# Performance work log

Hardware: AMD Instinct MI355X
Metric: run time of the kernel (lower is better)

The kernel has to match this reference:

```python
import jax, jax.numpy as jnp
import numpy as np

HIDDEN_DIM = 2048
CODE_DIM = 256
CODEBOOK_SIZE = 512
FC_DIMS = [1024, 512]
BATCH = 16384
EPS = 1e-5
NEG_SLOPE = 0.01  # PyTorch LeakyReLU default


def _linear_init(key, fan_in, fan_out):
    # kaiming_uniform_(a=sqrt(3)) ~= U(-1/sqrt(fan_in), 1/sqrt(fan_in)) scaled; use uniform bound
    bound = 1.0 / np.sqrt(fan_in)
    return jax.random.uniform(key, (fan_in, fan_out), jnp.float32, -bound, bound)


def setup_inputs() -> dict:
    key = jax.random.key(0)
    ks = jax.random.split(key, 16)
    h = jax.random.normal(ks[0], (BATCH, HIDDEN_DIM), jnp.float32)
    # encoder: Linear(2048->1024, no bias), BN, LReLU, Linear(1024->512, no bias), BN, LReLU, Linear(512->256, bias)
    enc_w1 = _linear_init(ks[1], HIDDEN_DIM, FC_DIMS[0])
    enc_bn1_g = jnp.ones((FC_DIMS[0],), jnp.float32)
    enc_bn1_b = jnp.zeros((FC_DIMS[0],), jnp.float32)
    enc_w2 = _linear_init(ks[2], FC_DIMS[0], FC_DIMS[1])
    enc_bn2_g = jnp.ones((FC_DIMS[1],), jnp.float32)
    enc_bn2_b = jnp.zeros((FC_DIMS[1],), jnp.float32)
    enc_w3 = _linear_init(ks[3], FC_DIMS[1], CODE_DIM)
    enc_b3 = jax.random.uniform(ks[4], (CODE_DIM,), jnp.float32, -1/np.sqrt(FC_DIMS[1]), 1/np.sqrt(FC_DIMS[1]))
    # codebook: NearestEmbed weight shape (code_dim, codebook_size)
    codebook = jax.random.normal(ks[5], (CODE_DIM, CODEBOOK_SIZE), jnp.float32)
    # decoder: Linear(256->512, no bias), BN, LReLU, Linear(512->1024, no bias), BN, LReLU, Linear(1024->2048, bias)
    dec_w1 = _linear_init(ks[6], CODE_DIM, FC_DIMS[1])
    dec_bn1_g = jnp.ones((FC_DIMS[1],), jnp.float32)
    dec_bn1_b = jnp.zeros((FC_DIMS[1],), jnp.float32)
    dec_w2 = _linear_init(ks[7], FC_DIMS[1], FC_DIMS[0])
    dec_bn2_g = jnp.ones((FC_DIMS[0],), jnp.float32)
    dec_bn2_b = jnp.zeros((FC_DIMS[0],), jnp.float32)
    dec_w3 = _linear_init(ks[8], FC_DIMS[0], HIDDEN_DIM)
    dec_b3 = jax.random.uniform(ks[9], (HIDDEN_DIM,), jnp.float32, -1/np.sqrt(FC_DIMS[0]), 1/np.sqrt(FC_DIMS[0]))
    return dict(h=h, enc_w1=enc_w1, enc_bn1_g=enc_bn1_g, enc_bn1_b=enc_bn1_b,
                enc_w2=enc_w2, enc_bn2_g=enc_bn2_g, enc_bn2_b=enc_bn2_b,
                enc_w3=enc_w3, enc_b3=enc_b3, codebook=codebook,
                dec_w1=dec_w1, dec_bn1_g=dec_bn1_g, dec_bn1_b=dec_bn1_b,
                dec_w2=dec_w2, dec_bn2_g=dec_bn2_g, dec_bn2_b=dec_bn2_b,
                dec_w3=dec_w3, dec_b3=dec_b3)


def _bn(x, g, b):
    # BatchNorm1d, training mode: biased batch variance, eps=1e-5
    mu = jnp.mean(x, axis=0)
    var = jnp.var(x, axis=0)
    return (x - mu) * jax.lax.rsqrt(var + EPS) * g + b


def _lrelu(x):
    return jnp.where(x >= 0, x, NEG_SLOPE * x)


def _quantize(z_e, codebook):
    # nearest codebook entry; codebook is [code_dim, K]
    # dist[b,k] = ||z_e[b] - codebook[:,k]||^2 (expanded, drop constant ||z||^2 for argmin? keep full for clarity)
    d = (jnp.sum(z_e * z_e, axis=1, keepdims=True)
         - 2.0 * (z_e @ codebook)
         + jnp.sum(codebook * codebook, axis=0)[None, :])  # [B, K]
    idx = jnp.argmin(d, axis=1)  # [B]
    z_q = codebook.T[idx]        # [B, code_dim]
    return z_q, idx


def reference(h, enc_w1, enc_bn1_g, enc_bn1_b, enc_w2, enc_bn2_g, enc_bn2_b,
              enc_w3, enc_b3, codebook,
              dec_w1, dec_bn1_g, dec_bn1_b, dec_w2, dec_bn2_g, dec_bn2_b,
              dec_w3, dec_b3):
    # encoder
    x = _lrelu(_bn(h @ enc_w1, enc_bn1_g, enc_bn1_b))
    x = _lrelu(_bn(x @ enc_w2, enc_bn2_g, enc_bn2_b))
    z_e = x @ enc_w3 + enc_b3  # [B, code_dim]
    # nearest-embed quantization with straight-through estimator
    z_q_raw, code_indices = _quantize(z_e, codebook)
    z_q = z_e + jax.lax.stop_gradient(z_q_raw - z_e)
    # decoder
    y = _lrelu(_bn(z_q @ dec_w1, dec_bn1_g, dec_bn1_b))
    y = _lrelu(_bn(y @ dec_w2, dec_bn2_g, dec_bn2_b))
    h_recon = y @ dec_w3 + dec_b3  # [B, hidden_dim]
    return z_e, z_q, h_recon, code_indices
```

## Files before the change

kernel.cpp:

```cpp
#include <hip/hip_runtime.h>
#include <hip/hip_fp16.h>
#include <cstdint>
#include <cstddef>

typedef _Float16 f16;
typedef _Float16 half8 __attribute__((ext_vector_type(8)));
typedef _Float16 half4 __attribute__((ext_vector_type(4)));
typedef float floatx4 __attribute__((ext_vector_type(4)));

static constexpr size_t NB  = 16384;
static constexpr size_t DH  = 2048;
static constexpr size_t F1  = 1024;
static constexpr size_t F2  = 512;
static constexpr size_t CD  = 256;
static constexpr size_t KCB = 512;

static constexpr size_t ZE_OFF  = 0;
static constexpr size_t ZQ_OFF  = NB * CD;
static constexpr size_t HR_OFF  = 2 * NB * CD;
static constexpr size_t IDX_OFF = 2 * NB * CD + NB * DH;

static constexpr size_t O_HH   = 0;
static constexpr size_t O_HL   = O_HH + NB * DH * 2;
static constexpr size_t R1_END = O_HL + NB * DH * 2;

static constexpr size_t R_X1H = 0;
static constexpr size_t R_X1L = NB * F1 * 2;
static constexpr size_t R_X2F = 2 * NB * F1 * 2;
static constexpr size_t R_X2H = R_X2F + NB * F2 * 4;
static constexpr size_t R_X2L = R_X2H + NB * F2 * 2;
static constexpr size_t R_Y1F = 0;
static constexpr size_t R_Y1H = NB * F2 * 4;
static constexpr size_t R_Y2H = 0;

static constexpr size_t O_W1H = R1_END;
static constexpr size_t O_W1L = O_W1H + F1 * DH * 2;
static constexpr size_t O_W2H = O_W1L + F1 * DH * 2;
static constexpr size_t O_W2L = O_W2H + F2 * F1 * 2;
static constexpr size_t O_W3H = O_W2L + F2 * F1 * 2;
static constexpr size_t O_W3L = O_W3H + CD * F2 * 2;
static constexpr size_t O_CBH = O_W3L + CD * F2 * 2;
static constexpr size_t O_CBL = O_CBH + KCB * CD * 2;
static constexpr size_t O_DW1 = O_CBL + KCB * CD * 2;
static constexpr size_t O_DW2 = O_DW1 + F2 * CD * 2;
static constexpr size_t O_DW3 = O_DW2 + F1 * F2 * 2;
static constexpr size_t O_SUM = O_DW3 + DH * F1 * 2;
static constexpr size_t O_SQ  = O_SUM + 4 * 1024 * 8;
static constexpr size_t O_SC  = O_SQ + 4 * 1024 * 8;
static constexpr size_t O_SH  = O_SC + 4 * 1024 * 4;
static constexpr size_t O_CN  = O_SH + 4 * 1024 * 4;
static constexpr size_t R2    = (O_CN + 4096 + 255) & ~(size_t)255;
static constexpr size_t R2_X1F = R2;
static constexpr size_t R2_ZEH = R2;
static constexpr size_t R2_ZEL = R2 + NB * CD * 2;
static constexpr size_t R2_S   = R2 + 2 * NB * CD * 2;
static constexpr size_t R2_ZQH = R2_S + NB * KCB * 4;
static constexpr size_t R2_Y2F = R2;

#define GLLDS(src, dst)                                                          \
    __builtin_amdgcn_global_load_lds(                                            \
        (const __attribute__((address_space(1))) void*)(src),                    \
        (__attribute__((address_space(3))) void*)(dst), 16, 0, 0)

#define VMCNT(n)  asm volatile("s_waitcnt vmcnt(" #n ")" ::: "memory")
#define LGKMCNT0  asm volatile("s_waitcnt lgkmcnt(0)" ::: "memory")

template<int MW, bool BIAS, bool STATS, bool WSPLIT>
__global__ __launch_bounds__(512)
void gemm3_t(const f16* __restrict__ Ah_, const f16* __restrict__ Al_,
             const f16* __restrict__ Bh_, const f16* __restrict__ Bl_,
             float* __restrict__ C, const float* __restrict__ bias,
             double* __restrict__ ssum, double* __restrict__ ssq,
             f16* __restrict__ zeh, f16* __restrict__ zel,
             int M, int N, int K)
{
    constexpr int BM = MW * 32;
    __shared__ f16 lds[2][2][16384];
    const int tid  = threadIdx.x;
    const int lane = tid & 63;
    const int w    = tid >> 6;
    const int wr   = w >> 2, wn = w & 3;
    const int row0 = blockIdx.x * BM;
    const int col0 = blockIdx.y * 256;

    const int rr8 = lane >> 3;
    const int p   = (lane & 7) ^ rr8;
    const int rr  = w * 32 + rr8;
    const int arr = rr & (BM - 1);
    const f16* srcH = (p < 4) ? (Ah_ + (size_t)(row0 + arr) * K + p * 8)
                              : (Bh_ + (size_t)(col0 + rr) * K + (p - 4) * 8);
    const f16* srcL = (p < 4) ? (Al_ + (size_t)(row0 + arr) * K + p * 8)
                              : (Bl_ + (size_t)(col0 + rr) * K + (p - 4) * 8);
    const int dstBase = w * 32 * 64;
    const int KT = K >> 5;

    floatx4 acc[MW][4];
#pragma unroll
    for (int m = 0; m < MW; ++m)
#pragma unroll
        for (int n = 0; n < 4; ++n)
#pragma unroll
            for (int j = 0; j < 4; ++j) acc[m][n][j] = 0.f;

    const int l15 = lane & 15;
    const int sA  = lane >> 4;

#pragma unroll
    for (int j = 0; j < 4; ++j)
        GLLDS(srcH + (size_t)j * 8 * K, &lds[0][0][dstBase + j * 512]);
#pragma unroll
    for (int j = 0; j < 4; ++j)
        GLLDS(srcL + (size_t)j * 8 * K, &lds[0][1][dstBase + j * 512]);
    VMCNT(4);
    __builtin_amdgcn_s_barrier();

    half8 afh[MW], afl[MW], bfh[4], bfl[4];

    for (int kt = 0; kt < KT; ++kt) {
        const int cur = kt & 1, nxt = cur ^ 1;
        const int koff = (kt + 1 < KT ? kt + 1 : kt) << 5;
        const f16* plH = lds[cur][0];
        const f16* plL = lds[cur][1];

#pragma unroll
        for (int m = 0; m < MW; ++m) {
            const int rA = wr * (MW * 16) + m * 16 + l15;
            afh[m] = *(const half8*)(plH + rA * 64 + (((sA) ^ (rA & 7)) << 3));
        }
#pragma unroll
        for (int n = 0; n < 4; ++n) {
            const int rB = wn * 64 + n * 16 + l15;
            bfh[n] = *(const half8*)(plH + rB * 64 + (((4 + sA) ^ (rB & 7)) << 3));
        }
#pragma unroll
        for (int j = 0; j < 4; ++j)
            GLLDS(srcH + (size_t)j * 8 * K + koff, &lds[nxt][0][dstBase + j * 512]);
        VMCNT(4);
        __builtin_amdgcn_s_barrier();
        LGKMCNT0;
        __builtin_amdgcn_sched_barrier(0);
        __builtin_amdgcn_s_setprio(1);
#pragma unroll
        for (int m = 0; m < MW; ++m)
#pragma unroll
            for (int n = 0; n < 4; ++n)
                acc[m][n] = __builtin_amdgcn_mfma_f32_16x16x32_f16(afh[m], bfh[n], acc[m][n], 0, 0, 0);
        __builtin_amdgcn_s_setprio(0);
        __builtin_amdgcn_s_barrier();

#pragma unroll
        for (int n = 0; n < 4; ++n) {
            const int rB = wn * 64 + n * 16 + l15;
            bfl[n] = *(const half8*)(plL + rB * 64 + (((4 + sA) ^ (rB & 7)) << 3));
        }
#pragma unroll
        for (int j = 0; j < 2; ++j)
            GLLDS(srcL + (size_t)j * 8 * K + koff, &lds[nxt][1][dstBase + j * 512]);
        __builtin_amdgcn_s_barrier();
        LGKMCNT0;
        __builtin_amdgcn_sched_barrier(0);
        __builtin_amdgcn_s_setprio(1);
#pragma unroll
        for (int m = 0; m < MW; ++m)
#pragma unroll
            for (int n = 0; n < 4; ++n)
                acc[m][n] = __builtin_amdgcn_mfma_f32_16x16x32_f16(afh[m], bfl[n], acc[m][n], 0, 0, 0);
        __builtin_amdgcn_s_setprio(0);
        __builtin_amdgcn_s_barrier();

#pragma unroll
        for (int m = 0; m < MW; ++m) {
            const int rA = wr * (MW * 16) + m * 16 + l15;
            afl[m] = *(const half8*)(plL + rA * 64 + (((sA) ^ (rA & 7)) << 3));
        }
#pragma unroll
        for (int j = 2; j < 4; ++j)
            GLLDS(srcL + (size_t)j * 8 * K + koff, &lds[nxt][1][dstBase + j * 512]);
        VMCNT(4);
        __builtin_amdgcn_s_barrier();
        LGKMCNT0;
        __builtin_amdgcn_sched_barrier(0);
        __builtin_amdgcn_s_setprio(1);
#pragma unroll
        for (int m = 0; m < MW; ++m)
#pragma unroll
            for (int n = 0; n < 4; ++n)
                acc[m][n] = __builtin_amdgcn_mfma_f32_16x16x32_f16(afl[m], bfh[n], acc[m][n], 0, 0, 0);
        __builtin_amdgcn_s_setprio(0);
        __builtin_amdgcn_s_barrier();
    }
    VMCNT(0);

    const int cb0 = col0 + wn * 64;
    const int rb0 = row0 + wr * (MW * 16) + (lane >> 4) * 4;
#pragma unroll
    for (int n = 0; n < 4; ++n) {
        const int col = cb0 + n * 16 + l15;
        const float bv = BIAS ? bias[col] : 0.f;
        double sd = 0.0, sq = 0.0;
#pragma unroll
        for (int m = 0; m < MW; ++m) {
            const int row = rb0 + m * 16;
#pragma unroll
            for (int j = 0; j < 4; ++j) {
                const float v = acc[m][n][j] + bv;
                const size_t o = (size_t)(row + j) * N + col;
                C[o] = v;
                if (WSPLIT) {
                    const f16 hv = (f16)v;
                    zeh[o] = hv;
                    zel[o] = (f16)(v - (float)hv);
                }
                if (STATS) { sd += (double)v; sq += (double)v * (double)v; }
            }
        }
        if (STATS) {
            sd += __shfl_xor(sd, 16);
            sd += __shfl_xor(sd, 32);
            sq += __shfl_xor(sq, 16);
            sq += __shfl_xor(sq, 32);
            if (lane < 16) {
                atomicAdd(ssum + col, sd);
                atomicAdd(ssq + col, sq);
            }
        }
    }
}

template<bool BIAS, bool STATS>
__global__ __launch_bounds__(512)
void gemm1_8ph(const f16* __restrict__ A_, const f16* __restrict__ B_,
               float* __restrict__ C, const float* __restrict__ bias,
               double* __restrict__ ssum, double* __restrict__ ssq,
               int M, int N, int K)
{
    __shared__ f16 lds[3][16384];
    const int tid  = threadIdx.x;
    const int lane = tid & 63;
    const int w    = tid >> 6;
    const int wr   = w >> 2, wn = w & 3;
    const int row0 = blockIdx.x * 256;
    const int col0 = blockIdx.y * 256;

    const int rr8 = lane >> 3;
    const int p   = (lane & 7) ^ rr8;
    const int rr  = w * 32 + rr8;
    const f16* srcH = (p < 4) ? (A_ + (size_t)(row0 + rr) * K + p * 8)
                              : (B_ + (size_t)(col0 + rr) * K + (p - 4) * 8);
    const int dstBase = w * 32 * 64;
    const int KT = K >> 5;

    floatx4 acc[8][4];
#pragma unroll
    for (int m = 0; m < 8; ++m)
#pragma unroll
        for (int n = 0; n < 4; ++n)
#pragma unroll
            for (int j = 0; j < 4; ++j) acc[m][n][j] = 0.f;

    const int l15 = lane & 15;
    const int sA  = lane >> 4;

#pragma unroll
    for (int j = 0; j < 4; ++j)
        GLLDS(srcH + (size_t)j * 8 * K, &lds[0][dstBase + j * 512]);
    {
        const int k1 = (KT > 1 ? 1 : 0) << 5;
#pragma unroll
        for (int j = 0; j < 4; ++j)
            GLLDS(srcH + (size_t)j * 8 * K + k1, &lds[1][dstBase + j * 512]);
    }
    VMCNT(4);
    __builtin_amdgcn_s_barrier();

    half8 afh[8], bfh[4];

    for (int kt = 0; kt < KT; ++kt) {
        const int cur = kt % 3, tgt = (kt + 2) % 3;
        const int koff = (kt + 2 < KT ? kt + 2 : KT - 1) << 5;
        const f16* plH = lds[cur];

#pragma unroll
        for (int m = 0; m < 8; ++m) {
            const int rA = wr * 128 + m * 16 + l15;
            afh[m] = *(const half8*)(plH + rA * 64 + (((sA) ^ (rA & 7)) << 3));
        }
#pragma unroll
        for (int n = 0; n < 4; ++n) {
            const int rB = wn * 64 + n * 16 + l15;
            bfh[n] = *(const half8*)(plH + rB * 64 + (((4 + sA) ^ (rB & 7)) << 3));
        }
#pragma unroll
        for (int j = 0; j < 2; ++j)
            GLLDS(srcH + (size_t)j * 8 * K + koff, &lds[tgt][dstBase + j * 512]);
        __builtin_amdgcn_s_barrier();
        LGKMCNT0;
        __builtin_amdgcn_sched_barrier(0);
        __builtin_amdgcn_s_setprio(1);
#pragma unroll
        for (int m = 0; m < 8; ++m)
#pragma unroll
            for (int n = 0; n < 2; ++n)
                acc[m][n] = __builtin_amdgcn_mfma_f32_16x16x32_f16(afh[m], bfh[n], acc[m][n], 0, 0, 0);
        __builtin_amdgcn_s_setprio(0);
        __builtin_amdgcn_s_barrier();

#pragma unroll
        for (int j = 2; j < 4; ++j)
            GLLDS(srcH + (size_t)j * 8 * K + koff, &lds[tgt][dstBase + j * 512]);
        VMCNT(4);
        __builtin_amdgcn_s_barrier();
        __builtin_amdgcn_s_setprio(1);
#pragma unroll
        for (int m = 0; m < 8; ++m)
#pragma unroll
            for (int n = 2; n < 4; ++n)
                acc[m][n] = __builtin_amdgcn_mfma_f32_16x16x32_f16(afh[m], bfh[n], acc[m][n], 0, 0, 0);
        __builtin_amdgcn_s_setprio(0);
        __builtin_amdgcn_s_barrier();
    }
    VMCNT(0);

    const int cb0 = col0 + wn * 64;
    const int rb0 = row0 + wr * 128 + (lane >> 4) * 4;
#pragma unroll
    for (int n = 0; n < 4; ++n) {
        const int col = cb0 + n * 16 + l15;
        const float bv = BIAS ? bias[col] : 0.f;
        double sd = 0.0, sq = 0.0;
#pragma unroll
        for (int m = 0; m < 8; ++m) {
            const int row = rb0 + m * 16;
#pragma unroll
            for (int j = 0; j < 4; ++j) {
                const float v = acc[m][n][j] + bv;
                C[(size_t)(row + j) * N + col] = v;
                if (STATS) { sd += (double)v; sq += (double)v * (double)v; }
            }
        }
        if (STATS) {
            sd += __shfl_xor(sd, 16);
            sd += __shfl_xor(sd, 32);
            sq += __shfl_xor(sq, 16);
            sq += __shfl_xor(sq, 32);
            if (lane < 16) {
                atomicAdd(ssum + col, sd);
                atomicAdd(ssq + col, sq);
            }
        }
    }
}

__global__ void split_f32(const float* __restrict__ X, f16* __restrict__ hi,
                          f16* __restrict__ lo, size_t n4)
{
    const size_t stride = (size_t)gridDim.x * blockDim.x;
    for (size_t i = (size_t)blockIdx.x * blockDim.x + threadIdx.x; i < n4; i += stride) {
        const floatx4 x = ((const floatx4*)X)[i];
        half4 h, l;
#pragma unroll
        for (int j = 0; j < 4; ++j) {
            const float v = x[j];
            const f16 hv = (f16)v;
            h[j] = hv;
            l[j] = (f16)(v - (float)hv);
        }
        ((half4*)hi)[i] = h;
        ((half4*)lo)[i] = l;
    }
}

template<bool SPLIT>
__global__ void bn_apply(const float* __restrict__ X, const float* __restrict__ scale,
                         const float* __restrict__ shift, f16* __restrict__ Yhi,
                         f16* __restrict__ Ylo, size_t n4, int Nmask)
{
    const size_t stride = (size_t)gridDim.x * blockDim.x;
    for (size_t i = (size_t)blockIdx.x * blockDim.x + threadIdx.x; i < n4; i += stride) {
        const floatx4 x = ((const floatx4*)X)[i];
        const int col = (int)((i * 4) & (size_t)Nmask);
        half4 h, l;
#pragma unroll
        for (int j = 0; j < 4; ++j) {
            float v = x[j] * scale[col + j] + shift[col + j];
            v = v >= 0.f ? v : 0.01f * v;
            const f16 hv = (f16)v;
            h[j] = hv;
            if (SPLIT) l[j] = (f16)(v - (float)hv);
        }
        ((half4*)Yhi)[i] = h;
        if (SPLIT) ((half4*)Ylo)[i] = l;
    }
}

__global__ void bn_finalize(const double* __restrict__ ssum, const double* __restrict__ ssq,
                            const float* __restrict__ g, const float* __restrict__ b,
                            float* __restrict__ scale, float* __restrict__ shift, int N)
{
    const int j = blockIdx.x * blockDim.x + threadIdx.x;
    if (j < N) {
        const double inv = 1.0 / (double)NB;
        const double mean = ssum[j] * inv;
        const double var  = ssq[j] * inv - mean * mean;
        const double sc   = (double)g[j] / sqrt(var + 1e-5);
        scale[j] = (float)sc;
        shift[j] = (float)((double)b[j] - mean * sc);
    }
}

template<bool SPLIT>
__global__ void transpose_split(const float* __restrict__ W, f16* __restrict__ Thi,
                                f16* __restrict__ Tlo, int K, int N)
{
    __shared__ float tile[32][33];
    const int x = threadIdx.x;
    const int y = threadIdx.y;
    const int nt = blockIdx.x * 32;
    const int kt = blockIdx.y * 32;
#pragma unroll
    for (int i = 0; i < 32; i += 8)
        tile[y + i][x] = W[(size_t)(kt + y + i) * N + nt + x];
    __syncthreads();
#pragma unroll
    for (int i = 0; i < 32; i += 8) {
        const float v = tile[x][y + i];
        const size_t o = (size_t)(nt + y + i) * K + kt + x;
        const f16 hv = (f16)v;
        Thi[o] = hv;
        if (SPLIT) Tlo[o] = (f16)(v - (float)hv);
    }
}

__global__ void cnorm_kernel(const float* __restrict__ cb, float* __restrict__ cn)
{
    const int k = blockIdx.x * blockDim.x + threadIdx.x;
    if (k < (int)KCB) {
        double s = 0.0;
        for (int d = 0; d < (int)CD; ++d) {
            const float v = cb[(size_t)d * KCB + k];
            s += (double)v * v;
        }
        cn[k] = (float)s;
    }
}

__global__ void argmin_gather(const float* __restrict__ S, const float* __restrict__ cn,
                              const float* __restrict__ cb, float* __restrict__ zq,
                              float* __restrict__ idx_out, f16* __restrict__ zqh)
{
    const int lane = threadIdx.x & 63;
    const int row  = blockIdx.x * 4 + (threadIdx.x >> 6);
    const float* Sr = S + (size_t)row * KCB;
    float best = 3.4e38f;
    int bi = 0;
#pragma unroll
    for (int i = 0; i < 8; ++i) {
        const int k = lane + 64 * i;
        const float d = cn[k] - 2.f * Sr[k];
        if (d < best) { best = d; bi = k; }
    }
#pragma unroll
    for (int off = 32; off > 0; off >>= 1) {
        const float ob = __shfl_xor(best, off);
        const int   oi = __shfl_xor(bi, off);
        if (ob < best || (ob == best && oi < bi)) { best = ob; bi = oi; }
    }
    if (lane == 0) idx_out[row] = (float)bi;
#pragma unroll
    for (int i = 0; i < 4; ++i) {
        const int d = lane + 64 * i;
        const float v = cb[(size_t)d * KCB + bi];
        zq[(size_t)row * CD + d]  = v;
        zqh[(size_t)row * CD + d] = (f16)v;
    }
}

extern "C" void kernel_launch(void* const* d_in, const int* in_sizes, int n_in,
                              void* d_out, int out_size, void* d_ws, size_t ws_size,
                              hipStream_t stream)
{
    (void)in_sizes; (void)n_in; (void)out_size; (void)ws_size;
    const float* h   = (const float*)d_in[0];
    const float* ew1 = (const float*)d_in[1];
    const float* bg1 = (const float*)d_in[2];
    const float* bb1 = (const float*)d_in[3];
    const float* ew2 = (const float*)d_in[4];
    const float* bg2 = (const float*)d_in[5];
    const float* bb2 = (const float*)d_in[6];
    const float* ew3 = (const float*)d_in[7];
    const float* eb3 = (const float*)d_in[8];
    const float* cb  = (const float*)d_in[9];
    const float* dw1 = (const float*)d_in[10];
    const float* dg1 = (const float*)d_in[11];
    const float* db1 = (const float*)d_in[12];
    const float* dw2 = (const float*)d_in[13];
    const float* dg2 = (const float*)d_in[14];
    const float* db2 = (const float*)d_in[15];
    const float* dw3 = (const float*)d_in[16];
    const float* db3 = (const float*)d_in[17];

    char* ws = (char*)d_ws;
    float* out = (float*)d_out;

    f16* Hh  = (f16*)(ws + O_HH);
    f16* Hl  = (f16*)(ws + O_HL);
    f16* W1h = (f16*)(ws + O_W1H);
    f16* W1l = (f16*)(ws + O_W1L);
    f16* W2h = (f16*)(ws + O_W2H);
    f16* W2l = (f16*)(ws + O_W2L);
    f16* W3h = (f16*)(ws + O_W3H);
    f16* W3l = (f16*)(ws + O_W3L);
    f16* CBh = (f16*)(ws + O_CBH);
    f16* CBl = (f16*)(ws + O_CBL);
    f16* D1t = (f16*)(ws + O_DW1);
    f16* D2t = (f16*)(ws + O_DW2);
    f16* D3t = (f16*)(ws + O_DW3);
    double* sum0 = (double*)(ws + O_SUM);
    double* sq0  = (double*)(ws + O_SQ);
    float* sc0 = (float*)(ws + O_SC);
    float* sh0 = (float*)(ws + O_SH);
    float* cn  = (float*)(ws + O_CN);

    float* X1f = (float*)(ws + R2_X1F);
    f16*  X1h = (f16*)(ws + R_X1H);
    f16*  X1l = (f16*)(ws + R_X1L);
    float* X2f = (float*)(ws + R_X2F);
    f16*  X2h = (f16*)(ws + R_X2H);
    f16*  X2l = (f16*)(ws + R_X2L);
    f16*  Zeh = (f16*)(ws + R2_ZEH);
    f16*  Zel = (f16*)(ws + R2_ZEL);
    float* Sb  = (float*)(ws + R2_S);
    f16*  Zqh = (f16*)(ws + R2_ZQH);
    float* Y1f = (float*)(ws + R_Y1F);
    f16*  Y1h = (f16*)(ws + R_Y1H);
    float* Y2f = (float*)(ws + R2_Y2F);
    f16*  Y2h = (f16*)(ws + R_Y2H);

    hipMemsetAsync(ws + O_SUM, 0, 4 * 1024 * 8 * 2, stream);

    split_f32<<<2048, 256, 0, stream>>>(h, Hh, Hl, NB * DH / 4);
    transpose_split<true ><<<dim3(F1 / 32, DH / 32), dim3(32, 8), 0, stream>>>(ew1, W1h, W1l, DH, F1);
    transpose_split<true ><<<dim3(F2 / 32, F1 / 32), dim3(32, 8), 0, stream>>>(ew2, W2h, W2l, F1, F2);
    transpose_split<true ><<<dim3(CD / 32, F2 / 32), dim3(32, 8), 0, stream>>>(ew3, W3h, W3l, F2, CD);
    transpose_split<true ><<<dim3(KCB / 32, CD / 32), dim3(32, 8), 0, stream>>>(cb, CBh, CBl, CD, KCB);
    transpose_split<false><<<dim3(F2 / 32, CD / 32), dim3(32, 8), 0, stream>>>(dw1, D1t, nullptr, CD, F2);
    transpose_split<false><<<dim3(F1 / 32, F2 / 32), dim3(32, 8), 0, stream>>>(dw2, D2t, nullptr, F2, F1);
    transpose_split<false><<<dim3(DH / 32, F1 / 32), dim3(32, 8), 0, stream>>>(dw3, D3t, nullptr, F1, DH);

    gemm3_t<8, false, true, false><<<dim3(NB / 256, F1 / 256), 512, 0, stream>>>(
        Hh, Hl, W1h, W1l, X1f, nullptr, sum0, sq0, nullptr, nullptr, NB, F1, DH);
    bn_finalize<<<4, 256, 0, stream>>>(sum0, sq0, bg1, bb1, sc0, sh0, F1);
    bn_apply<true><<<2048, 256, 0, stream>>>(X1f, sc0, sh0, X1h, X1l, NB * F1 / 4, (int)F1 - 1);

    gemm3_t<4, false, true, false><<<dim3(NB / 128, F2 / 256), 512, 0, stream>>>(
        X1h, X1l, W2h, W2l, X2f, nullptr, sum0 + 1024, sq0 + 1024, nullptr, nullptr, NB, F2, F1);
    bn_finalize<<<2, 256, 0, stream>>>(sum0 + 1024, sq0 + 1024, bg2, bb2, sc0 + 1024, sh0 + 1024, F2);
    bn_apply<true><<<2048, 256, 0, stream>>>(X2f, sc0 + 1024, sh0 + 1024, X2h, X2l, NB * F2 / 4, (int)F2 - 1);

    gemm3_t<4, true, false, true><<<dim3(NB / 128, CD / 256), 512, 0, stream>>>(
        X2h, X2l, W3h, W3l, out + ZE_OFF, eb3, nullptr, nullptr, Zeh, Zel, NB, CD, F2);

    cnorm_kernel<<<2, 256, 0, stream>>>(cb, cn);
    gemm3_t<4, false, false, false><<<dim3(NB / 128, KCB / 256), 512, 0, stream>>>(
        Zeh, Zel, CBh, CBl, Sb, nullptr, nullptr, nullptr, nullptr, nullptr, NB, KCB, CD);
    argmin_gather<<<NB / 4, 256, 0, stream>>>(Sb, cn, cb, out + ZQ_OFF, out + IDX_OFF, Zqh);

    gemm1_8ph<false, true><<<dim3(NB / 256, F2 / 256), 512, 0, stream>>>(
        Zqh, D1t, Y1f, nullptr, sum0 + 2048, sq0 + 2048, NB, F2, CD);
    bn_finalize<<<2, 256, 0, stream>>>(sum0 + 2048, sq0 + 2048, dg1, db1, sc0 + 2048, sh0 + 2048, F2);
    bn_apply<false><<<2048, 256, 0, stream>>>(Y1f, sc0 + 2048, sh0 + 2048, Y1h, nullptr, NB * F2 / 4, (int)F2 - 1);

    gemm1_8ph<false, true><<<dim3(NB / 256, F1 / 256), 512, 0, stream>>>(
        Y1h, D2t, Y2f, nullptr, sum0 + 3072, sq0 + 3072, NB, F1, F2);
    bn_finalize<<<4, 256, 0, stream>>>(sum0 + 3072, sq0 + 3072, dg2, db2, sc0 + 3072, sh0 + 3072, F1);
    bn_apply<false><<<2048, 256, 0, stream>>>(Y2f, sc0 + 3072, sh0 + 3072, Y2h, nullptr, NB * F1 / 4, (int)F1 - 1);

    gemm1_8ph<true, false><<<dim3(NB / 256, DH / 256), 512, 0, stream>>>(
        Y2h, D3t, out + HR_OFF, db3, nullptr, nullptr, NB, DH, F1);
}
```

Before: 613.7 us.

## Restructure GEMM pipelines with fewer barriers, XCD-aware tile remap, templated row tiles

Both GEMM kernels drop intermediate barriers and collapse the phased MFMA loops. The global-to-LDS prefetch for a whole stage is now issued at once, and its vmcnt wait moves after the MFMAs so the loads overlap compute. A workgroup-ID remap spreads consecutive tiles across the 8 XCDs, aiming at better L2 locality. The decoder's single-precision GEMM becomes templated on rows per tile, and the first decoder layer uses 128-row tiles for more blocks. The risk is less latency hiding between phases and possible LDS race hazards if the barrier removal is not fully safe.

```diff
diff --git a/kernel.cpp b/kernel.cpp
--- a/kernel.cpp
+++ b/kernel.cpp
@@ -65,6 +65,15 @@
 #define VMCNT(n)  asm volatile("s_waitcnt vmcnt(" #n ")" ::: "memory")
 #define LGKMCNT0  asm volatile("s_waitcnt lgkmcnt(0)" ::: "memory")
 
+__device__ __forceinline__ void xcd_tile(int gx, int BM, int& row0, int& col0)
+{
+    int id = blockIdx.x + gx * blockIdx.y;
+    const int nwg = gx * gridDim.y;
+    id = (id & 7) * (nwg >> 3) + (id >> 3);
+    row0 = (id % gx) * BM;
+    col0 = (id / gx) * 256;
+}
+
 template<int MW, bool BIAS, bool STATS, bool WSPLIT>
 __global__ __launch_bounds__(512)
 void gemm3_t(const f16* __restrict__ Ah_, const f16* __restrict__ Al_,
@@ -80,8 +89,8 @@
     const int lane = tid & 63;
     const int w    = tid >> 6;
     const int wr   = w >> 2, wn = w & 3;
-    const int row0 = blockIdx.x * BM;
-    const int col0 = blockIdx.y * 256;
+    int row0, col0;
+    xcd_tile(gridDim.x, BM, row0, col0);
 
     const int rr8 = lane >> 3;
     const int p   = (lane & 7) ^ rr8;
@@ -135,8 +144,6 @@
 #pragma unroll
         for (int j = 0; j < 4; ++j)
             GLLDS(srcH + (size_t)j * 8 * K + koff, &lds[nxt][0][dstBase + j * 512]);
-        VMCNT(4);
-        __builtin_amdgcn_s_barrier();
         LGKMCNT0;
         __builtin_amdgcn_sched_barrier(0);
         __builtin_amdgcn_s_setprio(1);
@@ -146,6 +153,7 @@
             for (int n = 0; n < 4; ++n)
                 acc[m][n] = __builtin_amdgcn_mfma_f32_16x16x32_f16(afh[m], bfh[n], acc[m][n], 0, 0, 0);
         __builtin_amdgcn_s_setprio(0);
+        VMCNT(4);
         __builtin_amdgcn_s_barrier();
 
 #pragma unroll
@@ -154,9 +162,13 @@
             bfl[n] = *(const half8*)(plL + rB * 64 + (((4 + sA) ^ (rB & 7)) << 3));
         }
 #pragma unroll
-        for (int j = 0; j < 2; ++j)
+        for (int m = 0; m < MW; ++m) {
+            const int rA = wr * (MW * 16) + m * 16 + l15;
+            afl[m] = *(const half8*)(plL + rA * 64 + (((sA) ^ (rA & 7)) << 3));
+        }
+#pragma unroll
+        for (int j = 0; j < 4; ++j)
             GLLDS(srcL + (size_t)j * 8 * K + koff, &lds[nxt][1][dstBase + j * 512]);
-        __builtin_amdgcn_s_barrier();
         LGKMCNT0;
         __builtin_amdgcn_sched_barrier(0);
         __builtin_amdgcn_s_setprio(1);
@@ -165,28 +177,13 @@
 #pragma unroll
             for (int n = 0; n < 4; ++n)
                 acc[m][n] = __builtin_amdgcn_mfma_f32_16x16x32_f16(afh[m], bfl[n], acc[m][n], 0, 0, 0);
-        __builtin_amdgcn_s_setprio(0);
-        __builtin_amdgcn_s_barrier();
-
-#pragma unroll
-        for (int m = 0; m < MW; ++m) {
-            const int rA = wr * (MW * 16) + m * 16 + l15;
-            afl[m] = *(const half8*)(plL + rA * 64 + (((sA) ^ (rA & 7)) << 3));
-        }
-#pragma unroll
-        for (int j = 2; j < 4; ++j)
-            GLLDS(srcL + (size_t)j * 8 * K + koff, &lds[nxt][1][dstBase + j * 512]);
-        VMCNT(4);
-        __builtin_amdgcn_s_barrier();
-        LGKMCNT0;
-        __builtin_amdgcn_sched_barrier(0);
-        __builtin_amdgcn_s_setprio(1);
 #pragma unroll
         for (int m = 0; m < MW; ++m)
 #pragma unroll
             for (int n = 0; n < 4; ++n)
                 acc[m][n] = __builtin_amdgcn_mfma_f32_16x16x32_f16(afl[m], bfh[n], acc[m][n], 0, 0, 0);
         __builtin_amdgcn_s_setprio(0);
+        VMCNT(4);
         __builtin_amdgcn_s_barrier();
     }
     VMCNT(0);
@@ -227,32 +224,34 @@
     }
 }
 
-template<bool BIAS, bool STATS>
+template<int MW, bool BIAS, bool STATS>
 __global__ __launch_bounds__(512)
-void gemm1_8ph(const f16* __restrict__ A_, const f16* __restrict__ B_,
-               float* __restrict__ C, const float* __restrict__ bias,
-               double* __restrict__ ssum, double* __restrict__ ssq,
-               int M, int N, int K)
-{
+void gemm1_t(const f16* __restrict__ A_, const f16* __restrict__ B_,
+             float* __restrict__ C, const float* __restrict__ bias,
+             double* __restrict__ ssum, double* __restrict__ ssq,
+             int M, int N, int K)
+{
+    constexpr int BM = MW * 32;
     __shared__ f16 lds[3][16384];
     const int tid  = threadIdx.x;
     const int lane = tid & 63;
     const int w    = tid >> 6;
     const int wr   = w >> 2, wn = w & 3;
-    const int row0 = blockIdx.x * 256;
-    const int col0 = blockIdx.y * 256;
+    int row0, col0;
+    xcd_tile(gridDim.x, BM, row0, col0);
 
     const int rr8 = lane >> 3;
     const int p   = (lane & 7) ^ rr8;
     const int rr  = w * 32 + rr8;
-    const f16* srcH = (p < 4) ? (A_ + (size_t)(row0 + rr) * K + p * 8)
+    const int arr = rr & (BM - 1);
+    const f16* srcH = (p < 4) ? (A_ + (size_t)(row0 + arr) * K + p * 8)
                               : (B_ + (size_t)(col0 + rr) * K + (p - 4) * 8);
     const int dstBase = w * 32 * 64;
     const int KT = K >> 5;
 
-    floatx4 acc[8][4];
-#pragma unroll
-    for (int m = 0; m < 8; ++m)
+    floatx4 acc[MW][4];
+#pragma unroll
+    for (int m = 0; m < MW; ++m)
 #pragma unroll
         for (int n = 0; n < 4; ++n)
 #pragma unroll
@@ -273,7 +272,7 @@
     VMCNT(4);
     __builtin_amdgcn_s_barrier();
 
-    half8 afh[8], bfh[4];
+    half8 afh[MW], bfh[4];
 
     for (int kt = 0; kt < KT; ++kt) {
         const int cur = kt % 3, tgt = (kt + 2) % 3;
@@ -281,8 +280,8 @@
         const f16* plH = lds[cur];
 
 #pragma unroll
-        for (int m = 0; m < 8; ++m) {
-            const int rA = wr * 128 + m * 16 + l15;
+        for (int m = 0; m < MW; ++m) {
+            const int rA = wr * (MW * 16) + m * 16 + l15;
             afh[m] = *(const half8*)(plH + rA * 64 + (((sA) ^ (rA & 7)) << 3));
         }
 #pragma unroll
@@ -291,45 +290,31 @@
             bfh[n] = *(const half8*)(plH + rB * 64 + (((4 + sA) ^ (rB & 7)) << 3));
         }
 #pragma unroll
-        for (int j = 0; j < 2; ++j)
+        for (int j = 0; j < 4; ++j)
             GLLDS(srcH + (size_t)j * 8 * K + koff, &lds[tgt][dstBase + j * 512]);
-        __builtin_amdgcn_s_barrier();
         LGKMCNT0;
         __builtin_amdgcn_sched_barrier(0);
         __builtin_amdgcn_s_setprio(1);
 #pragma unroll
-        for (int m = 0; m < 8; ++m)
-#pragma unroll
-            for (int n = 0; n < 2; ++n)
+        for (int m = 0; m < MW; ++m)
+#pragma unroll
+            for (int n = 0; n < 4; ++n)
                 acc[m][n] = __builtin_amdgcn_mfma_f32_16x16x32_f16(afh[m], bfh[n], acc[m][n], 0, 0, 0);
         __builtin_amdgcn_s_setprio(0);
-        __builtin_amdgcn_s_barrier();
-
-#pragma unroll
-        for (int j = 2; j < 4; ++j)
-            GLLDS(srcH + (size_t)j * 8 * K + koff, &lds[tgt][dstBase + j * 512]);
         VMCNT(4);
         __builtin_amdgcn_s_barrier();
-        __builtin_amdgcn_s_setprio(1);
-#pragma unroll
-        for (int m = 0; m < 8; ++m)
-#pragma unroll
-            for (int n = 2; n < 4; ++n)
-                acc[m][n] = __builtin_amdgcn_mfma_f32_16x16x32_f16(afh[m], bfh[n], acc[m][n], 0, 0, 0);
-        __builtin_amdgcn_s_setprio(0);
-        __builtin_amdgcn_s_barrier();
     }
     VMCNT(0);
 
     const int cb0 = col0 + wn * 64;
-    const int rb0 = row0 + wr * 128 + (lane >> 4) * 4;
+    const int rb0 = row0 + wr * (MW * 16) + (lane >> 4) * 4;
 #pragma unroll
     for (int n = 0; n < 4; ++n) {
         const int col = cb0 + n * 16 + l15;
         const float bv = BIAS ? bias[col] : 0.f;
         double sd = 0.0, sq = 0.0;
 #pragma unroll
-        for (int m = 0; m < 8; ++m) {
+        for (int m = 0; m < MW; ++m) {
             const int row = rb0 + m * 16;
 #pragma unroll
             for (int j = 0; j < 4; ++j) {
@@ -565,16 +550,16 @@
         Zeh, Zel, CBh, CBl, Sb, nullptr, nullptr, nullptr, nullptr, nullptr, NB, KCB, CD);
     argmin_gather<<<NB / 4, 256, 0, stream>>>(Sb, cn, cb, out + ZQ_OFF, out + IDX_OFF, Zqh);
 
-    gemm1_8ph<false, true><<<dim3(NB / 256, F2 / 256), 512, 0, stream>>>(
+    gemm1_t<4, false, true><<<dim3(NB / 128, F2 / 256), 512, 0, stream>>>(
         Zqh, D1t, Y1f, nullptr, sum0 + 2048, sq0 + 2048, NB, F2, CD);
     bn_finalize<<<2, 256, 0, stream>>>(sum0 + 2048, sq0 + 2048, dg1, db1, sc0 + 2048, sh0 + 2048, F2);
     bn_apply<false><<<2048, 256, 0, stream>>>(Y1f, sc0 + 2048, sh0 + 2048, Y1h, nullptr, NB * F2 / 4, (int)F2 - 1);
 
-    gemm1_8ph<false, true><<<dim3(NB / 256, F1 / 256), 512, 0, stream>>>(
+    gemm1_t<8, false, true><<<dim3(NB / 256, F1 / 256), 512, 0, stream>>>(
         Y1h, D2t, Y2f, nullptr, sum0 + 3072, sq0 + 3072, NB, F1, F2);
     bn_finalize<<<4, 256, 0, stream>>>(sum0 + 3072, sq0 + 3072, dg2, db2, sc0 + 3072, sh0 + 3072, F1);
     bn_apply<false><<<2048, 256, 0, stream>>>(Y2f, sc0 + 3072, sh0 + 3072, Y2h, nullptr, NB * F1 / 4, (int)F1 - 1);
 
-    gemm1_8ph<true, false><<<dim3(NB / 256, DH / 256), 512, 0, stream>>>(
+    gemm1_t<8, true, false><<<dim3(NB / 256, DH / 256), 512, 0, stream>>>(
         Y2h, D3t, out + HR_OFF, db3, nullptr, nullptr, NB, DH, F1);
 }
```

Measured after the change: 598.4 us. 2.5% less time.
